# Kernel optimization log

Hardware: AMD Instinct MI355X
Metric: run time of the kernel (lower is better)

Reference implementation:

```python
import jax, jax.numpy as jnp
import numpy as np

D_MODEL = 1024
N_HEADS = 16
D_K = D_MODEL // N_HEADS
B, S = 2, 2048


def setup_inputs() -> dict:
    key = jax.random.key(0)
    ks = jax.random.split(key, 11)
    def lin(kw, kb, fan_in):
        bound = 1.0 / np.sqrt(fan_in)
        W = jax.random.uniform(kw, (fan_in, D_MODEL), jnp.float32, -bound, bound)
        b = jax.random.uniform(kb, (D_MODEL,), jnp.float32, -bound, bound)
        return W, b
    Wq, bq = lin(ks[0], ks[1], D_MODEL)
    Wk, bk = lin(ks[2], ks[3], D_MODEL)
    Wv, bv = lin(ks[4], ks[5], D_MODEL)
    Wo, bo = lin(ks[6], ks[7], D_MODEL)
    q = jax.random.normal(ks[8], (B, S, D_MODEL), jnp.float32)
    k = jax.random.normal(ks[9], (B, S, D_MODEL), jnp.float32)
    v = jax.random.normal(ks[10], (B, S, D_MODEL), jnp.float32)
    return {"q": q, "k": k, "v": v,
            "Wq": Wq, "bq": bq, "Wk": Wk, "bk": bk,
            "Wv": Wv, "bv": bv, "Wo": Wo, "bo": bo}


def reference(q, k, v, Wq, bq, Wk, bk, Wv, bv, Wo, bo):
    Bz, Sq, _ = q.shape
    def split_heads(x):  # [B,S,D] -> [B,H,S,d_k]
        return x.reshape(x.shape[0], x.shape[1], N_HEADS, D_K).transpose(0, 2, 1, 3)
    qh = split_heads(q @ Wq + bq)
    kh = split_heads(k @ Wk + bk)
    vh = split_heads(v @ Wv + bv)
    scores = jnp.einsum("bhqd,bhkd->bhqk", qh, kh) / jnp.sqrt(jnp.float32(D_K))
    attn = jax.nn.softmax(scores, axis=-1)
    out = jnp.einsum("bhqk,bhkd->bhqd", attn, vh)
    out = out.transpose(0, 2, 1, 3).reshape(Bz, Sq, D_MODEL)
    return out @ Wo + bo
```

## Files before the change

### kernel.cpp

```cpp
#include <hip/hip_runtime.h>
#include <hip/hip_bf16.h>
#include <stdint.h>

typedef __bf16 bf16;
typedef __bf16 bf16x8 __attribute__((ext_vector_type(8)));
typedef __bf16 bf16x4 __attribute__((ext_vector_type(4)));
typedef float  f32x4  __attribute__((ext_vector_type(4)));
typedef float  f32x16 __attribute__((ext_vector_type(16)));
typedef uint32_t u32;

#define MFMA16(a,b,c) __builtin_amdgcn_mfma_f32_16x16x32_bf16((a),(b),(c),0,0,0)
#define MFMA32(a,b,c) __builtin_amdgcn_mfma_f32_32x32x16_bf16((a),(b),(c),0,0,0)

#define QSCL 0.1803368801111204f

__device__ __forceinline__ u32 sx32(u32 x) {
    return (u32)__shfl_xor((int)x, 32, 64);
}
__device__ __forceinline__ float swapred_max(float v) {
    return fmaxf(v, __builtin_bit_cast(float, sx32(__builtin_bit_cast(u32, v))));
}
__device__ __forceinline__ float swapred_sum(float v) {
    return v + __builtin_bit_cast(float, sx32(__builtin_bit_cast(u32, v)));
}
__device__ __forceinline__ u32 pkbf(float lo, float hi) {
    union { bf16 h[2]; u32 u; } un;
    un.h[0] = (bf16)lo; un.h[1] = (bf16)hi;
    return un.u;
}
__device__ __forceinline__ void pack_frags(const float* p, int hi, bf16x8& f0, bf16x8& f1) {
    u32 k01 = pkbf(p[0],  p[1]),  k23 = pkbf(p[2],  p[3]);
    u32 k45 = pkbf(p[4],  p[5]),  k67 = pkbf(p[6],  p[7]);
    u32 k89 = pkbf(p[8],  p[9]),  kab = pkbf(p[10], p[11]);
    u32 kcd = pkbf(p[12], p[13]), kef = pkbf(p[14], p[15]);
    u32 x01 = sx32(k01), x23 = sx32(k23), x45 = sx32(k45), x67 = sx32(k67);
    u32 x89 = sx32(k89), xab = sx32(kab), xcd = sx32(kcd), xef = sx32(kef);
    union { u32 w[4]; bf16x8 v; } u0, u1;
    u0.w[0] = hi ? x45 : k01;  u0.w[1] = hi ? x67 : k23;
    u0.w[2] = hi ? k45 : x01;  u0.w[3] = hi ? k67 : x23;
    u1.w[0] = hi ? xcd : k89;  u1.w[1] = hi ? xef : kab;
    u1.w[2] = hi ? kcd : x89;  u1.w[3] = hi ? kef : xab;
    f0 = u0.v; f1 = u1.v;
}

__device__ __forceinline__ void transpose_body(const float* __restrict__ W, bf16* __restrict__ Wt,
                                               float scale, int n0, int k0) {
    __shared__ bf16 t[64][65];
    for (int i = 0; i < 16; ++i) {
        int idx = threadIdx.x + i * 256, r = idx >> 6, c = idx & 63;
        t[r][c] = (bf16)(W[(size_t)(k0 + r) * 1024 + n0 + c] * scale);
    }
    __syncthreads();
    for (int i = 0; i < 16; ++i) {
        int idx = threadIdx.x + i * 256, r = idx >> 6, c = idx & 63;
        Wt[(size_t)(n0 + r) * 1024 + k0 + c] = t[c][r];
    }
}
__global__ __launch_bounds__(256) void k_transpose_w(const float* __restrict__ W,
                                                     bf16* __restrict__ Wt, float scale) {
    transpose_body(W, Wt, scale, blockIdx.x * 64, blockIdx.y * 64);
}
__global__ __launch_bounds__(256) void k_transpose_w4(const float* __restrict__ Wq, const float* __restrict__ Wk,
                                                      const float* __restrict__ Wv, const float* __restrict__ Wo,
                                                      bf16* __restrict__ Wtq, bf16* __restrict__ Wtk,
                                                      bf16* __restrict__ Wtv, bf16* __restrict__ Wto) {
    int z = blockIdx.z;
    const float* W = (z == 0) ? Wq : (z == 1) ? Wk : (z == 2) ? Wv : Wo;
    bf16* Wt = (z == 0) ? Wtq : (z == 1) ? Wtk : (z == 2) ? Wtv : Wto;
    transpose_body(W, Wt, (z == 0) ? QSCL : 1.0f, blockIdx.x * 64, blockIdx.y * 64);
}

template <int F32_IS_A>
__device__ __forceinline__ void gemm_pipe(const float* __restrict__ P32, const bf16* __restrict__ P16,
                                          const float* __restrict__ bias, float bscale,
                                          void* __restrict__ Cp, int out_mode, int m0, int n0,
                                          bf16 (*S32)[64], bf16 (*L16)[64]) {
    const int tid = threadIdx.x;
    const int wid = tid >> 6, lane = tid & 63, lg = lane >> 4, lm = lane & 15;
    const int wr = wid >> 1, wc = wid & 1;
    const int grow = tid >> 3, gcol = (tid & 7) << 3;
    const int r32base = F32_IS_A ? m0 : n0;
    const int r16base = F32_IS_A ? n0 : m0;

    f32x4 acc[4][4] = {};
    float4 rA[4][2];

    auto issue32 = [&](int kt) {
#pragma unroll
        for (int p = 0; p < 4; ++p) {
            const float* src = P32 + (size_t)(r32base + p * 32 + grow) * 1024 + (kt << 6) + gcol;
            rA[p][0] = *(const float4*)src;
            rA[p][1] = *(const float4*)(src + 4);
        }
    };
    auto write32 = [&](int buf) {
#pragma unroll
        for (int p = 0; p < 4; ++p) {
            bf16x8 w = {(bf16)rA[p][0].x, (bf16)rA[p][0].y, (bf16)rA[p][0].z, (bf16)rA[p][0].w,
                        (bf16)rA[p][1].x, (bf16)rA[p][1].y, (bf16)rA[p][1].z, (bf16)rA[p][1].w};
            *(bf16x8*)&S32[buf * 128 + p * 32 + grow][gcol] = w;
        }
    };
    auto stage16 = [&](int kt, int buf) {
#pragma unroll
        for (int p = 0; p < 4; ++p)
            __builtin_amdgcn_global_load_lds(
                (const __attribute__((address_space(1))) void*)(P16 + (size_t)(r16base + p * 32 + grow) * 1024 + (kt << 6) + gcol),
                (__attribute__((address_space(3))) void*)(&L16[buf * 128 + p * 32 + wid * 8][0]), 16, 0, 0);
    };

    issue32(0);
    stage16(0, 0);
    write32(0);
    __syncthreads();

    int buf = 0;
#pragma unroll 1
    for (int kt = 0; kt < 16; ++kt) {
        if (kt < 15) {
            issue32(kt + 1);
            stage16(kt + 1, buf ^ 1);
        }
#pragma unroll
        for (int kk = 0; kk < 2; ++kk) {
            bf16x8 a[4], b[4];
#pragma unroll
            for (int i = 0; i < 4; ++i) {
                if constexpr (F32_IS_A)
                    a[i] = *(const bf16x8*)&S32[buf * 128 + wr * 64 + i * 16 + lm][kk * 32 + lg * 8];
                else
                    a[i] = *(const bf16x8*)&L16[buf * 128 + wr * 64 + i * 16 + lm][kk * 32 + lg * 8];
            }
#pragma unroll
            for (int j = 0; j < 4; ++j) {
                if constexpr (F32_IS_A)
                    b[j] = *(const bf16x8*)&L16[buf * 128 + wc * 64 + j * 16 + lm][kk * 32 + lg * 8];
                else
                    b[j] = *(const bf16x8*)&S32[buf * 128 + wc * 64 + j * 16 + lm][kk * 32 + lg * 8];
            }
#pragma unroll
            for (int i = 0; i < 4; ++i)
#pragma unroll
                for (int j = 0; j < 4; ++j) acc[i][j] = MFMA16(a[i], b[j], acc[i][j]);
        }
        if (kt < 15) write32(buf ^ 1);
        __syncthreads();
        buf ^= 1;
    }

    for (int i = 0; i < 4; ++i) {
        for (int j = 0; j < 4; ++j) {
            int col = n0 + wc * 64 + j * 16 + lm;
            for (int q = 0; q < 4; ++q) {
                int row = m0 + wr * 64 + i * 16 + lg * 4 + q;
                if (out_mode == 0) {
                    float val = acc[i][j][q] + bscale * bias[col];
                    int bb = row >> 11, s = row & 2047, h = col >> 6, d = col & 63;
                    ((bf16*)Cp)[(((size_t)bb * 16 + h) * 2048 + s) * 64 + d] = (bf16)val;
                } else {
                    float val = acc[i][j][q] + bias[row];
                    size_t idx = (((size_t)(col >> 11) * 16 + (row >> 6)) * 64 + (row & 63)) * 2048 + (col & 2047);
                    ((bf16*)Cp)[idx] = (bf16)val;
                }
            }
        }
    }
}

__device__ __forceinline__ void tile_decode(int r, int& m0, int& n0) {
    int xcd = r & 7, slot = (r >> 3) & 3, n = (r >> 5) & 7;
    m0 = (xcd * 4 + slot) * 128;
    n0 = n * 128;
}
__device__ __forceinline__ void tile_decode_vt(int r, int& m0, int& n0) {
    int xcd = r & 7, loc = r >> 3;
    int nslot = loc & 3, m = loc >> 2;
    n0 = (xcd * 4 + nslot) * 128;
    m0 = m * 128;
}

__global__ __launch_bounds__(256, 2) void k_gemm_proj(const float* __restrict__ A,
                                                      const bf16* __restrict__ Bt,
                                                      const float* __restrict__ bias, float bscale,
                                                      void* __restrict__ Cp) {
    __shared__ bf16 S32[256][64];
    __shared__ bf16 L16[256][64];
    int m0, n0;
    tile_decode(blockIdx.x, m0, n0);
    gemm_pipe<1>(A, Bt, bias, bscale, Cp, 0, m0, n0, S32, L16);
}

__global__ __launch_bounds__(256, 2) void k_gemm_vt(const bf16* __restrict__ Wtv,
                                                    const float* __restrict__ v,
                                                    const float* __restrict__ bias,
                                                    bf16* __restrict__ Vtb) {
    __shared__ bf16 S32[256][64];
    __shared__ bf16 L16[256][64];
    int m0, n0;
    tile_decode_vt(blockIdx.x, m0, n0);
    gemm_pipe<0>(v, Wtv, bias, 1.0f, (void*)Vtb, 2, m0, n0, S32, L16);
}

__global__ __launch_bounds__(256, 2) void k_gemm_qkv(const float* __restrict__ q, const float* __restrict__ k,
                                                     const float* __restrict__ v,
                                                     const bf16* __restrict__ Wtq, const bf16* __restrict__ Wtk,
                                                     const bf16* __restrict__ Wtv,
                                                     const float* __restrict__ bq, const float* __restrict__ bk,
                                                     const float* __restrict__ bv,
                                                     bf16* __restrict__ Qb, bf16* __restrict__ Kb,
                                                     bf16* __restrict__ Vtb) {
    __shared__ bf16 S32[256][64];
    __shared__ bf16 L16[256][64];
    int l = blockIdx.x, z = l >> 8, r = l & 255;
    int m0, n0;
    if (z == 2) {
        tile_decode_vt(r, m0, n0);
        gemm_pipe<0>(v, Wtv, bv, 1.0f, (void*)Vtb, 2, m0, n0, S32, L16);
    } else {
        tile_decode(r, m0, n0);
        const float* A  = (z == 0) ? q : k;
        const bf16* Bt  = (z == 0) ? Wtq : Wtk;
        const float* bias = (z == 0) ? bq : bk;
        float bscale = (z == 0) ? QSCL : 1.0f;
        bf16* Cp = (z == 0) ? Qb : Kb;
        gemm_pipe<1>(A, Bt, bias, bscale, (void*)Cp, 0, m0, n0, S32, L16);
    }
}

__global__ __launch_bounds__(256, 4) void k_gemm_out(const bf16* __restrict__ A,
                                                     const bf16* __restrict__ Bt,
                                                     const float* __restrict__ bias,
                                                     float* __restrict__ C) {
    __shared__ bf16 As[128][64];
    __shared__ bf16 Bs[64][64];
    const int tid = threadIdx.x;
    const int wid = tid >> 6, lane = tid & 63, lg = lane >> 4, lm = lane & 15;
    const int grow = tid >> 3, gcol = (tid & 7) << 3;
    const int r = blockIdx.x;
    const int xcd = r & 7, loc = r >> 3;
    const int mslot = loc & 3, n = loc >> 2;
    const int m0 = (xcd * 4 + mslot) * 128, n0 = n * 64;

    f32x4 acc[2][4] = {};

    for (int kt = 0; kt < 16; ++kt) {
        const int k0 = kt << 6;
        __syncthreads();
#pragma unroll
        for (int p = 0; p < 4; ++p)
            __builtin_amdgcn_global_load_lds(
                (const __attribute__((address_space(1))) void*)(A + (size_t)(m0 + p * 32 + grow) * 1024 + k0 + gcol),
                (__attribute__((address_space(3))) void*)(&As[p * 32 + wid * 8][0]), 16, 0, 0);
#pragma unroll
        for (int p = 0; p < 2; ++p)
            __builtin_amdgcn_global_load_lds(
                (const __attribute__((address_space(1))) void*)(Bt + (size_t)(n0 + p * 32 + grow) * 1024 + k0 + gcol),
                (__attribute__((address_space(3))) void*)(&Bs[p * 32 + wid * 8][0]), 16, 0, 0);
        __syncthreads();
#pragma unroll
        for (int kk = 0; kk < 2; ++kk) {
            bf16x8 a[2], b[4];
#pragma unroll
            for (int i = 0; i < 2; ++i) a[i] = *(const bf16x8*)&As[wid * 32 + i * 16 + lm][kk * 32 + lg * 8];
#pragma unroll
            for (int j = 0; j < 4; ++j) b[j] = *(const bf16x8*)&Bs[j * 16 + lm][kk * 32 + lg * 8];
#pragma unroll
            for (int i = 0; i < 2; ++i)
#pragma unroll
                for (int j = 0; j < 4; ++j) acc[i][j] = MFMA16(a[i], b[j], acc[i][j]);
        }
    }

    for (int i = 0; i < 2; ++i) {
        for (int j = 0; j < 4; ++j) {
            int col = n0 + j * 16 + lm;
            float bv = bias[col];
            for (int q = 0; q < 4; ++q) {
                int row = m0 + wid * 32 + i * 16 + lg * 4 + q;
                C[(size_t)row * 1024 + col] = acc[i][j][q] + bv;
            }
        }
    }
}

__global__ __launch_bounds__(512, 2) void k_attn(const bf16* __restrict__ Q,
                                                 const bf16* __restrict__ Kb,
                                                 const bf16* __restrict__ Vt,
                                                 bf16* __restrict__ Out) {
    __shared__ bf16 Ks[2][64 * 64];
    __shared__ bf16 Vs[2][64 * 64];
    const int tid = threadIdx.x;
    const int wid = tid >> 6, lane = tid & 63;
    const int lm = lane & 31, hi = lane >> 5;
    const int bid = blockIdx.x;
    const int bh = bid & 31, qt = bid >> 5;
    const int bb = bh >> 4, h = bh & 15;
    const int qrow = qt * 256 + wid * 32 + lm;
    const size_t qk_base = (size_t)bh * (2048 * 64);
    const size_t vt_base = (size_t)bh * (64 * 2048);

    const int srow = tid >> 3, sc8 = tid & 7;
    const int cse = (sc8 ^ (srow & 7)) * 8;
    const bf16* kstage = Kb + qk_base + (size_t)srow * 64 + cse;
    const bf16* vstage = Vt + vt_base + (size_t)srow * 2048 + cse;
    const int ldsoff = wid * 1024;

    bf16x8 qf[4];
    {
        const bf16* qp = Q + qk_base + (size_t)qrow * 64 + hi * 8;
#pragma unroll
        for (int f = 0; f < 4; ++f) qf[f] = *(const bf16x8*)(qp + f * 16);
    }

    f32x16 O0 = {}, O1 = {};
    float mrow = -1e30f, lsum = 0.f;

    const int swz = (lm & 7);

    __builtin_amdgcn_global_load_lds(
        (const __attribute__((address_space(1))) void*)(kstage),
        (__attribute__((address_space(3))) void*)((char*)&Ks[0][0] + ldsoff), 16, 0, 0);
    __builtin_amdgcn_global_load_lds(
        (const __attribute__((address_space(1))) void*)(vstage),
        (__attribute__((address_space(3))) void*)((char*)&Vs[0][0] + ldsoff), 16, 0, 0);
    __syncthreads();

    int cur = 0;
#pragma unroll 1
    for (int kt = 0; kt < 32; ++kt) {
        if (kt + 1 < 32) {
            __builtin_amdgcn_global_load_lds(
                (const __attribute__((address_space(1))) void*)(kstage + (size_t)(kt + 1) * 4096),
                (__attribute__((address_space(3))) void*)((char*)&Ks[cur ^ 1][0] + ldsoff), 16, 0, 0);
            __builtin_amdgcn_global_load_lds(
                (const __attribute__((address_space(1))) void*)(vstage + (size_t)(kt + 1) * 64),
                (__attribute__((address_space(3))) void*)((char*)&Vs[cur ^ 1][0] + ldsoff), 16, 0, 0);
        }

        const char* Ksc = (const char*)&Ks[cur][0];
        const char* Vsc = (const char*)&Vs[cur][0];

        bf16x8 kf0[4], kf1[4];
#pragma unroll
        for (int f = 0; f < 4; ++f) {
            int ch = (f << 1) | hi;
            kf0[f] = *(const bf16x8*)(Ksc + lm * 128 + ((ch ^ swz) << 4));
            kf1[f] = *(const bf16x8*)(Ksc + (lm + 32) * 128 + ((ch ^ swz) << 4));
        }
        bf16x8 vf0[4], vf1[4];
#pragma unroll
        for (int ks = 0; ks < 4; ++ks) {
            int ch = (ks << 1) | hi;
            vf0[ks] = *(const bf16x8*)(Vsc + lm * 128 + ((ch ^ swz) << 4));
            vf1[ks] = *(const bf16x8*)(Vsc + (lm + 32) * 128 + ((ch ^ swz) << 4));
        }

        f32x16 s0 = {}, s1 = {};
#pragma unroll
        for (int f = 0; f < 4; ++f) {
            s0 = MFMA32(kf0[f], qf[f], s0);
            s1 = MFMA32(kf1[f], qf[f], s1);
        }

        float pe0[16], pe1[16];
#pragma unroll
        for (int r = 0; r < 16; ++r) pe0[r] = __builtin_amdgcn_exp2f(s0[r] - mrow);
#pragma unroll
        for (int r = 0; r < 16; ++r) pe1[r] = __builtin_amdgcn_exp2f(s1[r] - mrow);

        float t8[8];
#pragma unroll
        for (int r = 0; r < 8; ++r)
            t8[r] = fmaxf(fmaxf(s0[r], s0[r + 8]), fmaxf(s1[r], s1[r + 8]));
#pragma unroll
        for (int st = 4; st; st >>= 1)
#pragma unroll
            for (int r = 0; r < st; ++r) t8[r] = fmaxf(t8[r], t8[r + st]);
        float pm = swapred_max(t8[0]);

        if (!__all(pm <= mrow + 8.0f)) {
            float mnew = fmaxf(mrow, pm);
            float corr = __builtin_amdgcn_exp2f(mrow - mnew);
            lsum *= corr;
            O0 *= corr;
            O1 *= corr;
            mrow = mnew;
#pragma unroll
            for (int r = 0; r < 16; ++r) pe0[r] = __builtin_amdgcn_exp2f(s0[r] - mrow);
#pragma unroll
            for (int r = 0; r < 16; ++r) pe1[r] = __builtin_amdgcn_exp2f(s1[r] - mrow);
        }

        float u8[8];
#pragma unroll
        for (int r = 0; r < 8; ++r) u8[r] = (pe0[r] + pe0[r + 8]) + (pe1[r] + pe1[r + 8]);
#pragma unroll
        for (int st = 4; st; st >>= 1)
#pragma unroll
            for (int r = 0; r < st; ++r) u8[r] = u8[r] + u8[r + st];
        lsum += u8[0];

        bf16x8 pf[4];
        pack_frags(pe0, hi, pf[0], pf[1]);
        pack_frags(pe1, hi, pf[2], pf[3]);

#pragma unroll
        for (int ks = 0; ks < 4; ++ks) {
            O0 = MFMA32(vf0[ks], pf[ks], O0);
            O1 = MFMA32(vf1[ks], pf[ks], O1);
        }

        __syncthreads();
        cur ^= 1;
    }

    float lrow = swapred_sum(lsum);
    float inv = 1.0f / lrow;
    bf16* op = Out + ((size_t)bb * 2048 + qrow) * 1024 + h * 64 + 4 * hi;
#pragma unroll
    for (int t = 0; t < 4; ++t) {
        bf16x4 w0, w1;
#pragma unroll
        for (int e = 0; e < 4; ++e) {
            w0[e] = (bf16)(O0[4 * t + e] * inv);
            w1[e] = (bf16)(O1[4 * t + e] * inv);
        }
        *(bf16x4*)(op + 8 * t)      = w0;
        *(bf16x4*)(op + 32 + 8 * t) = w1;
    }
}

extern "C" void kernel_launch(void* const* d_in, const int* in_sizes, int n_in,
                              void* d_out, int out_size, void* d_ws, size_t ws_size,
                              hipStream_t stream) {
    const float* q  = (const float*)d_in[0];
    const float* k  = (const float*)d_in[1];
    const float* v  = (const float*)d_in[2];
    const float* Wq = (const float*)d_in[3];
    const float* bq = (const float*)d_in[4];
    const float* Wk = (const float*)d_in[5];
    const float* bk = (const float*)d_in[6];
    const float* Wv = (const float*)d_in[7];
    const float* bv = (const float*)d_in[8];
    const float* Wo = (const float*)d_in[9];
    const float* bo = (const float*)d_in[10];

    char* ws = (char*)d_ws;
    const size_t MB = 1ull << 20;
    const dim3 twg(16, 16), blk(256);

    if (ws_size >= 40 * MB) {
        bf16* Wtq = (bf16*)(ws + 0 * MB);
        bf16* Wtk = (bf16*)(ws + 2 * MB);
        bf16* Wtv = (bf16*)(ws + 4 * MB);
        bf16* Wto = (bf16*)(ws + 6 * MB);
        bf16* Qb  = (bf16*)(ws + 8 * MB);
        bf16* Kb  = (bf16*)(ws + 16 * MB);
        bf16* Vtb = (bf16*)(ws + 24 * MB);
        bf16* AOb = (bf16*)(ws + 32 * MB);

        k_transpose_w4<<<dim3(16, 16, 4), blk, 0, stream>>>(Wq, Wk, Wv, Wo, Wtq, Wtk, Wtv, Wto);
        k_gemm_qkv<<<768, blk, 0, stream>>>(q, k, v, Wtq, Wtk, Wtv, bq, bk, bv, Qb, Kb, Vtb);
        k_attn<<<256, 512, 0, stream>>>(Qb, Kb, Vtb, AOb);
        k_gemm_out<<<512, blk, 0, stream>>>(AOb, Wto, bo, (float*)d_out);
    } else {
        bf16* Wt   = (bf16*)(ws + 0 * MB);
        bf16* Qb   = (bf16*)(ws + 2 * MB);
        bf16* Kb   = (bf16*)(ws + 10 * MB);
        bf16* Vtb  = (bf16*)(ws + 18 * MB);
        bf16* AOb  = (bf16*)(ws + 26 * MB);

        k_transpose_w<<<twg, blk, 0, stream>>>(Wq, Wt, QSCL);
        k_gemm_proj<<<256, blk, 0, stream>>>(q, Wt, bq, QSCL, (void*)Qb);
        k_transpose_w<<<twg, blk, 0, stream>>>(Wk, Wt, 1.0f);
        k_gemm_proj<<<256, blk, 0, stream>>>(k, Wt, bk, 1.0f, (void*)Kb);
        k_transpose_w<<<twg, blk, 0, stream>>>(Wv, Wt, 1.0f);
        k_gemm_vt<<<256, blk, 0, stream>>>(Wt, v, bv, Vtb);
        k_transpose_w<<<twg, blk, 0, stream>>>(Wo, Wt, 1.0f);
        k_attn<<<256, 512, 0, stream>>>(Qb, Kb, Vtb, AOb);
        k_gemm_out<<<512, blk, 0, stream>>>(AOb, Wt, bo, (float*)d_out);
    }
}
```

Measured before the change: 146.8 us.

## Pre-convert QKV inputs to bf16 and use 256x256-tile bf16 projection GEMM

A separate elementwise kernel now converts q, k and v from fp32 to bf16 in workspace. A new 512-thread projection GEMM then works on 256x256 tiles, staging both operands into double-buffered, swizzled LDS with direct global-to-LDS loads. It uses explicit waitcnt and barrier scheduling and raises MFMA priority around the math loops. The aim is more operand reuse per tile and no fp32-to-bf16 conversion inside the GEMM main loop. In exchange it adds an extra memory-bound pass over the activations, launches only 192 blocks, and needs a 64MB workspace for this path; the remaining global-to-LDS calls are only wrapped in a helper.

```diff
diff --git a/kernel.cpp b/kernel.cpp
--- a/kernel.cpp
+++ b/kernel.cpp
@@ -27,6 +27,11 @@
     union { bf16 h[2]; u32 u; } un;
     un.h[0] = (bf16)lo; un.h[1] = (bf16)hi;
     return un.u;
+}
+__device__ __forceinline__ void glds16(const bf16* src, bf16* ldsDst) {
+    __builtin_amdgcn_global_load_lds(
+        (const __attribute__((address_space(1))) void*)src,
+        (__attribute__((address_space(3))) void*)ldsDst, 16, 0, 0);
 }
 __device__ __forceinline__ void pack_frags(const float* p, int hi, bf16x8& f0, bf16x8& f1) {
     u32 k01 = pkbf(p[0],  p[1]),  k23 = pkbf(p[2],  p[3]);
@@ -43,6 +48,20 @@
     f0 = u0.v; f1 = u1.v;
 }
 
+__global__ __launch_bounds__(256) void k_cvt3(const float* __restrict__ a, const float* __restrict__ b,
+                                              const float* __restrict__ c,
+                                              bf16* __restrict__ x, bf16* __restrict__ y,
+                                              bf16* __restrict__ z) {
+    int i = blockIdx.x * 256 + threadIdx.x;
+    int t = i >> 20;
+    int r = (i & 1048575) << 2;
+    const float* s = (t == 0) ? a : ((t == 1) ? b : c);
+    bf16* d = (t == 0) ? x : ((t == 1) ? y : z);
+    float4 v = *(const float4*)&s[r];
+    bf16x4 w = {(bf16)v.x, (bf16)v.y, (bf16)v.z, (bf16)v.w};
+    *(bf16x4*)&d[r] = w;
+}
+
 __device__ __forceinline__ void transpose_body(const float* __restrict__ W, bf16* __restrict__ Wt,
                                                float scale, int n0, int k0) {
     __shared__ bf16 t[64][65];
@@ -68,6 +87,137 @@
     const float* W = (z == 0) ? Wq : (z == 1) ? Wk : (z == 2) ? Wv : Wo;
     bf16* Wt = (z == 0) ? Wtq : (z == 1) ? Wtk : (z == 2) ? Wtv : Wto;
     transpose_body(W, Wt, (z == 0) ? QSCL : 1.0f, blockIdx.x * 64, blockIdx.y * 64);
+}
+
+__device__ __forceinline__ void gemm256(const bf16* __restrict__ Ag, const bf16* __restrict__ Bg,
+                                        const float* __restrict__ bias, float bscale,
+                                        bf16* __restrict__ Cp, int m0, int n0, int out_mode,
+                                        bf16* As, bf16* Bs) {
+    const int tid = threadIdx.x;
+    const int wid = tid >> 6, lane = tid & 63;
+    const int lm = lane & 15, g = lane >> 4, swz = lane & 7;
+    const int wm = wid >> 2, wn = wid & 3;
+
+    const int rl8 = (lane >> 3) & 7;
+    const int lcs = (lane & 7) ^ rl8;
+    const bf16* Asrc = Ag + (size_t)(m0 + wid * 32 + rl8) * 1024 + lcs * 8;
+    const bf16* Bsrc = Bg + (size_t)(n0 + wid * 32 + rl8) * 1024 + lcs * 8;
+
+    f32x4 acc[8][4] = {};
+
+#define STAGE256(KT, S)                                                      \
+    do {                                                                     \
+        _Pragma("unroll")                                                    \
+        for (int j = 0; j < 4; ++j) {                                        \
+            glds16(Asrc + (size_t)j * 8192 + (KT) * 64,                      \
+                   As + (S) * 16384 + (wid * 4 + j) * 512);                  \
+            glds16(Bsrc + (size_t)j * 8192 + (KT) * 64,                      \
+                   Bs + (S) * 16384 + (wid * 4 + j) * 512);                  \
+        }                                                                    \
+    } while (0)
+
+    STAGE256(0, 0);
+    STAGE256(1, 1);
+    asm volatile("s_waitcnt vmcnt(8)" ::: "memory");
+    __builtin_amdgcn_s_barrier();
+
+#pragma unroll 1
+    for (int t = 0; t < 16; ++t) {
+        const int s = t & 1;
+        const bf16* Ab = As + s * 16384;
+        const bf16* Bb = Bs + s * 16384;
+
+        bf16x8 af[8][2], bfr[4][2];
+#pragma unroll
+        for (int mf = 0; mf < 8; ++mf) {
+            const bf16* rp = Ab + (wm * 128 + mf * 16 + lm) * 64;
+#pragma unroll
+            for (int ks = 0; ks < 2; ++ks)
+                af[mf][ks] = *(const bf16x8*)(rp + ((((ks * 4 + g) ^ swz)) << 3));
+        }
+#pragma unroll
+        for (int nf = 0; nf < 4; ++nf) {
+            const bf16* rp = Bb + (wn * 64 + nf * 16 + lm) * 64;
+#pragma unroll
+            for (int ks = 0; ks < 2; ++ks)
+                bfr[nf][ks] = *(const bf16x8*)(rp + ((((ks * 4 + g) ^ swz)) << 3));
+        }
+        __builtin_amdgcn_s_setprio(1);
+#pragma unroll
+        for (int mf = 0; mf < 8; ++mf)
+#pragma unroll
+            for (int nf = 0; nf < 4; ++nf)
+                acc[mf][nf] = MFMA16(af[mf][0], bfr[nf][0], acc[mf][nf]);
+        __builtin_amdgcn_s_setprio(0);
+        __builtin_amdgcn_sched_barrier(0);
+        asm volatile("s_waitcnt lgkmcnt(0)" ::: "memory");
+        __builtin_amdgcn_sched_barrier(0);
+        __builtin_amdgcn_s_barrier();
+
+        if (t + 2 < 16) STAGE256(t + 2, s);
+        __builtin_amdgcn_s_setprio(1);
+#pragma unroll
+        for (int mf = 0; mf < 8; ++mf)
+#pragma unroll
+            for (int nf = 0; nf < 4; ++nf)
+                acc[mf][nf] = MFMA16(af[mf][1], bfr[nf][1], acc[mf][nf]);
+        __builtin_amdgcn_s_setprio(0);
+        __builtin_amdgcn_sched_barrier(0);
+        if (t < 14)       asm volatile("s_waitcnt vmcnt(8)" ::: "memory");
+        else if (t == 14) asm volatile("s_waitcnt vmcnt(0)" ::: "memory");
+        __builtin_amdgcn_sched_barrier(0);
+        __builtin_amdgcn_s_barrier();
+    }
+#undef STAGE256
+
+#pragma unroll
+    for (int mf = 0; mf < 8; ++mf) {
+#pragma unroll
+        for (int nf = 0; nf < 4; ++nf) {
+            int col = n0 + wn * 64 + nf * 16 + lm;
+            for (int q = 0; q < 4; ++q) {
+                int row = m0 + wm * 128 + mf * 16 + g * 4 + q;
+                if (out_mode == 0) {
+                    float val = acc[mf][nf][q] + bscale * bias[col];
+                    int bb = row >> 11, sq = row & 2047, h = col >> 6, d = col & 63;
+                    Cp[(((size_t)bb * 16 + h) * 2048 + sq) * 64 + d] = (bf16)val;
+                } else {
+                    float val = acc[mf][nf][q] + bias[row];
+                    size_t idx = (((size_t)(col >> 11) * 16 + (row >> 6)) * 64 + (row & 63)) * 2048 + (col & 2047);
+                    Cp[idx] = (bf16)val;
+                }
+            }
+        }
+    }
+}
+
+__global__ __launch_bounds__(512, 2) void k_gemm_qkv8(const bf16* __restrict__ qc, const bf16* __restrict__ kc,
+                                                      const bf16* __restrict__ vc,
+                                                      const bf16* __restrict__ Wtq, const bf16* __restrict__ Wtk,
+                                                      const bf16* __restrict__ Wtv,
+                                                      const float* __restrict__ bq, const float* __restrict__ bk,
+                                                      const float* __restrict__ bv,
+                                                      bf16* __restrict__ Qb, bf16* __restrict__ Kb,
+                                                      bf16* __restrict__ Vtb) {
+    __shared__ bf16 As[2][16384];
+    __shared__ bf16 Bs[2][16384];
+    const int bid = blockIdx.x, z = bid >> 6, r = bid & 63;
+    const bf16 *Ag, *Bg;
+    const float* bias;
+    float bscale;
+    bf16* Cp;
+    int m0, n0, mode;
+    if (z == 2) {
+        Ag = Wtv; Bg = vc; bias = bv; bscale = 1.0f; Cp = Vtb;
+        m0 = (r & 3) * 256; n0 = (r >> 2) * 256; mode = 2;
+    } else if (z == 0) {
+        Ag = qc; Bg = Wtq; bias = bq; bscale = QSCL; Cp = Qb;
+        m0 = (r >> 2) * 256; n0 = (r & 3) * 256; mode = 0;
+    } else {
+        Ag = kc; Bg = Wtk; bias = bk; bscale = 1.0f; Cp = Kb;
+        m0 = (r >> 2) * 256; n0 = (r & 3) * 256; mode = 0;
+    }
+    gemm256(Ag, Bg, bias, bscale, Cp, m0, n0, mode, &As[0][0], &Bs[0][0]);
 }
 
 template <int F32_IS_A>
@@ -104,9 +254,8 @@
     auto stage16 = [&](int kt, int buf) {
 #pragma unroll
         for (int p = 0; p < 4; ++p)
-            __builtin_amdgcn_global_load_lds(
-                (const __attribute__((address_space(1))) void*)(P16 + (size_t)(r16base + p * 32 + grow) * 1024 + (kt << 6) + gcol),
-                (__attribute__((address_space(3))) void*)(&L16[buf * 128 + p * 32 + wid * 8][0]), 16, 0, 0);
+            glds16(P16 + (size_t)(r16base + p * 32 + grow) * 1024 + (kt << 6) + gcol,
+                   &L16[buf * 128 + p * 32 + wid * 8][0]);
     };
 
     issue32(0);
@@ -201,32 +350,6 @@
     gemm_pipe<0>(v, Wtv, bias, 1.0f, (void*)Vtb, 2, m0, n0, S32, L16);
 }
 
-__global__ __launch_bounds__(256, 2) void k_gemm_qkv(const float* __restrict__ q, const float* __restrict__ k,
-                                                     const float* __restrict__ v,
-                                                     const bf16* __restrict__ Wtq, const bf16* __restrict__ Wtk,
-                                                     const bf16* __restrict__ Wtv,
-                                                     const float* __restrict__ bq, const float* __restrict__ bk,
-                                                     const float* __restrict__ bv,
-                                                     bf16* __restrict__ Qb, bf16* __restrict__ Kb,
-                                                     bf16* __restrict__ Vtb) {
-    __shared__ bf16 S32[256][64];
-    __shared__ bf16 L16[256][64];
-    int l = blockIdx.x, z = l >> 8, r = l & 255;
-    int m0, n0;
-    if (z == 2) {
-        tile_decode_vt(r, m0, n0);
-        gemm_pipe<0>(v, Wtv, bv, 1.0f, (void*)Vtb, 2, m0, n0, S32, L16);
-    } else {
-        tile_decode(r, m0, n0);
-        const float* A  = (z == 0) ? q : k;
-        const bf16* Bt  = (z == 0) ? Wtq : Wtk;
-        const float* bias = (z == 0) ? bq : bk;
-        float bscale = (z == 0) ? QSCL : 1.0f;
-        bf16* Cp = (z == 0) ? Qb : Kb;
-        gemm_pipe<1>(A, Bt, bias, bscale, (void*)Cp, 0, m0, n0, S32, L16);
-    }
-}
-
 __global__ __launch_bounds__(256, 4) void k_gemm_out(const bf16* __restrict__ A,
                                                      const bf16* __restrict__ Bt,
                                                      const float* __restrict__ bias,
@@ -248,14 +371,10 @@
         __syncthreads();
 #pragma unroll
         for (int p = 0; p < 4; ++p)
-            __builtin_amdgcn_global_load_lds(
-                (const __attribute__((address_space(1))) void*)(A + (size_t)(m0 + p * 32 + grow) * 1024 + k0 + gcol),
-                (__attribute__((address_space(3))) void*)(&As[p * 32 + wid * 8][0]), 16, 0, 0);
+            glds16(A + (size_t)(m0 + p * 32 + grow) * 1024 + k0 + gcol, &As[p * 32 + wid * 8][0]);
 #pragma unroll
         for (int p = 0; p < 2; ++p)
-            __builtin_amdgcn_global_load_lds(
-                (const __attribute__((address_space(1))) void*)(Bt + (size_t)(n0 + p * 32 + grow) * 1024 + k0 + gcol),
-                (__attribute__((address_space(3))) void*)(&Bs[p * 32 + wid * 8][0]), 16, 0, 0);
+            glds16(Bt + (size_t)(n0 + p * 32 + grow) * 1024 + k0 + gcol, &Bs[p * 32 + wid * 8][0]);
         __syncthreads();
 #pragma unroll
         for (int kk = 0; kk < 2; ++kk) {
@@ -303,7 +422,7 @@
     const int cse = (sc8 ^ (srow & 7)) * 8;
     const bf16* kstage = Kb + qk_base + (size_t)srow * 64 + cse;
     const bf16* vstage = Vt + vt_base + (size_t)srow * 2048 + cse;
-    const int ldsoff = wid * 1024;
+    const int ldsoff = wid * 512;
 
     bf16x8 qf[4];
     {
@@ -317,24 +436,16 @@
 
     const int swz = (lm & 7);
 
-    __builtin_amdgcn_global_load_lds(
-        (const __attribute__((address_space(1))) void*)(kstage),
-        (__attribute__((address_space(3))) void*)((char*)&Ks[0][0] + ldsoff), 16, 0, 0);
-    __builtin_amdgcn_global_load_lds(
-        (const __attribute__((address_space(1))) void*)(vstage),
-        (__attribute__((address_space(3))) void*)((char*)&Vs[0][0] + ldsoff), 16, 0, 0);
+    glds16(kstage, &Ks[0][0] + ldsoff);
+    glds16(vstage, &Vs[0][0] + ldsoff);
     __syncthreads();
 
     int cur = 0;
 #pragma unroll 1
     for (int kt = 0; kt < 32; ++kt) {
         if (kt + 1 < 32) {
-            __builtin_amdgcn_global_load_lds(
-                (const __attribute__((address_space(1))) void*)(kstage + (size_t)(kt + 1) * 4096),
-                (__attribute__((address_space(3))) void*)((char*)&Ks[cur ^ 1][0] + ldsoff), 16, 0, 0);
-            __builtin_amdgcn_global_load_lds(
-                (const __attribute__((address_space(1))) void*)(vstage + (size_t)(kt + 1) * 64),
-                (__attribute__((address_space(3))) void*)((char*)&Vs[cur ^ 1][0] + ldsoff), 16, 0, 0);
+            glds16(kstage + (size_t)(kt + 1) * 4096, &Ks[cur ^ 1][0] + ldsoff);
+            glds16(vstage + (size_t)(kt + 1) * 64, &Vs[cur ^ 1][0] + ldsoff);
         }
 
         const char* Ksc = (const char*)&Ks[cur][0];
@@ -449,18 +560,22 @@
     const size_t MB = 1ull << 20;
     const dim3 twg(16, 16), blk(256);
 
-    if (ws_size >= 40 * MB) {
+    if (ws_size >= 64 * MB) {
         bf16* Wtq = (bf16*)(ws + 0 * MB);
         bf16* Wtk = (bf16*)(ws + 2 * MB);
         bf16* Wtv = (bf16*)(ws + 4 * MB);
         bf16* Wto = (bf16*)(ws + 6 * MB);
-        bf16* Qb  = (bf16*)(ws + 8 * MB);
-        bf16* Kb  = (bf16*)(ws + 16 * MB);
-        bf16* Vtb = (bf16*)(ws + 24 * MB);
-        bf16* AOb = (bf16*)(ws + 32 * MB);
+        bf16* qc  = (bf16*)(ws + 8 * MB);
+        bf16* kc  = (bf16*)(ws + 16 * MB);
+        bf16* vc  = (bf16*)(ws + 24 * MB);
+        bf16* Qb  = (bf16*)(ws + 32 * MB);
+        bf16* Kb  = (bf16*)(ws + 40 * MB);
+        bf16* Vtb = (bf16*)(ws + 48 * MB);
+        bf16* AOb = (bf16*)(ws + 56 * MB);
 
         k_transpose_w4<<<dim3(16, 16, 4), blk, 0, stream>>>(Wq, Wk, Wv, Wo, Wtq, Wtk, Wtv, Wto);
-        k_gemm_qkv<<<768, blk, 0, stream>>>(q, k, v, Wtq, Wtk, Wtv, bq, bk, bv, Qb, Kb, Vtb);
+        k_cvt3<<<12288, blk, 0, stream>>>(q, k, v, qc, kc, vc);
+        k_gemm_qkv8<<<192, 512, 0, stream>>>(qc, kc, vc, Wtq, Wtk, Wtv, bq, bk, bv, Qb, Kb, Vtb);
         k_attn<<<256, 512, 0, stream>>>(Qb, Kb, Vtb, AOb);
         k_gemm_out<<<512, blk, 0, stream>>>(AOb, Wto, bo, (float*)d_out);
     } else {
```

New measurement: 155.4 us. +5.9%, slower.
